# Kernel tuning notes

Measured on AMD Instinct MI355X. Metric: run time of the kernel, lower is better.

Reference implementation:

```python
import jax, jax.numpy as jnp
import numpy as np

B, L, NE, DOUT = 4, 4096, 64, 64
DI = 128          # backbone model dim (hardcoded d_inner in MambaDoc)
NL = 2            # num_layers
H = 2             # num_heads
N = 128           # state_dim
G = 1             # num_groups
CONV = 4          # conv_size
DIN = 2 * DI      # expand=2 -> 256 inner channels of the mixer
P = DIN // H      # headdim = 128
CCH = DIN + 2 * G * N      # 512 conv channels (x, B, C)
DPROJ = 2 * DIN + 2 * G * N + H  # 770 in_proj output width


def setup_inputs() -> dict:
    key = jax.random.key(0)
    ks = jax.random.split(key, 8)
    s = lambda k, shape, sc: (jax.random.normal(k, shape, jnp.float32) * sc)
    return {
        "x": s(ks[0], (B, L, NE), 1.0),
        "in_w": s(ks[1], (DI, NE), (1.0 / NE) ** 0.5),
        "in_b": jnp.zeros((DI,), jnp.float32),
        "out_w": s(ks[2], (DOUT, DI), (1.0 / DI) ** 0.5),
        "out_b": jnp.zeros((DOUT,), jnp.float32),
        "l_rms_w": jnp.ones((NL, DI), jnp.float32),
        "l_in_w": s(ks[3], (NL, DPROJ, DI), (1.0 / DI) ** 0.5),
        "conv_w": s(ks[4], (NL, CCH, CONV), (1.0 / CONV) ** 0.5),
        "conv_b": jnp.zeros((NL, CCH), jnp.float32),
        "dt_bias": s(ks[5], (NL, H), 0.1),
        "A_log": jnp.zeros((NL, H), jnp.float32),   # A = -exp(A_log) = -1
        "D_p": jnp.ones((NL, H), jnp.float32),
        "gnorm_w": jnp.ones((NL, DIN), jnp.float32),
        "l_out_w": s(ks[6], (NL, DI, DIN), (1.0 / DIN) ** 0.5),
        "fnorm_w": jnp.ones((DI,), jnp.float32),
    }


def _rms(x, w, eps=1e-5):
    return x * jax.lax.rsqrt(jnp.mean(x * x, -1, keepdims=True) + eps) * w


def _mamba_layer(x, rms_w, in_w, cw, cb, dtb, a_log, d, gnw, ow):
    # x: (B,L,DI)
    h = _rms(x, rms_w)
    zxbcdt = jnp.einsum("bld,ed->ble", h, in_w)  # (B,L,770)
    z, xBC, dt = jnp.split(zxbcdt, [DIN, DIN + CCH], axis=-1)
    # causal depthwise conv over time, conv_size taps
    xp = jnp.pad(xBC, ((0, 0), (CONV - 1, 0), (0, 0)))
    xc = cb + sum(xp[:, k:k + L, :] * cw[:, k] for k in range(CONV))
    xc = jax.nn.silu(xc)
    xs, Bm, Cm = jnp.split(xc, [DIN, DIN + G * N], axis=-1)
    xs = xs.reshape(B, L, H, P)
    dt = jax.nn.softplus(dt + dtb)                 # (B,L,H)
    dA = jnp.exp(dt * (-jnp.exp(a_log)))           # (B,L,H) discrete decay

    def step(hc, inp):
        dA_t, dt_t, x_t, B_t, C_t = inp  # (B,H),(B,H),(B,H,P),(B,N),(B,N)
        hc = hc * dA_t[:, :, None, None] + (dt_t[:, :, None] * x_t)[..., None] * B_t[:, None, None, :]
        y = jnp.einsum("bhpn,bn->bhp", hc, C_t)
        return hc, y

    h0 = jnp.zeros((B, H, P, N), x.dtype)
    seq = (jnp.moveaxis(dA, 1, 0), jnp.moveaxis(dt, 1, 0), jnp.moveaxis(xs, 1, 0),
           jnp.moveaxis(Bm, 1, 0), jnp.moveaxis(Cm, 1, 0))
    _, ys = jax.lax.scan(step, h0, seq)
    y = jnp.moveaxis(ys, 0, 1)                     # (B,L,H,P)
    y = y + xs * d[None, None, :, None]            # D skip connection
    y = _rms(y.reshape(B, L, DIN) * jax.nn.silu(z), gnw)  # gated RMSNorm
    return x + jnp.einsum("ble,de->bld", y, ow)


def reference(x, in_w, in_b, out_w, out_b, l_rms_w, l_in_w, conv_w, conv_b,
              dt_bias, A_log, D_p, gnorm_w, l_out_w, fnorm_w):
    xp = jnp.einsum("bln,dn->bld", x, in_w) + in_b
    h = xp
    for i in range(NL):
        h = _mamba_layer(h, l_rms_w[i], l_in_w[i], conv_w[i], conv_b[i],
                         dt_bias[i], A_log[i], D_p[i], gnorm_w[i], l_out_w[i])
    h = _rms(h, fnorm_w)            # backbone final norm
    out = xp + h                    # outer residual in MambaDoc.forward
    return jnp.einsum("bld,od->blo", out, out_w) + out_b
```

## Files before the change

### kernel.cpp

```cpp
#include <hip/hip_runtime.h>
#include <cstddef>
#include <cstdint>


#define LSEQ 4096
#define MTOK 16384

typedef unsigned short u16;
typedef _Float16 f16x8 __attribute__((ext_vector_type(8)));
typedef float f32x4 __attribute__((ext_vector_type(4)));

__device__ __forceinline__ u16 f2h(float x) {
    return __builtin_bit_cast(u16, (_Float16)x);
}
__device__ __forceinline__ float h2f(u16 u) {
    return (float)__builtin_bit_cast(_Float16, u);
}
__device__ __forceinline__ float silu_f(float x) { return x / (1.f + __expf(-x)); }

__device__ __forceinline__ void async_lds16(const void* g, void* l) {
    __builtin_amdgcn_global_load_lds(
        (const __attribute__((address_space(1))) unsigned int*)g,
        (__attribute__((address_space(3))) unsigned int*)l, 16, 0, 0);
}

__device__ __forceinline__ void cvt16(
    const float* __restrict__ in, u16* __restrict__ out, int g)
{
    float4 v = *(const float4*)&in[(size_t)g * 4];
    union { u16 u[4]; uint2 q; } pk;
    pk.u[0] = f2h(v.x); pk.u[1] = f2h(v.y);
    pk.u[2] = f2h(v.z); pk.u[3] = f2h(v.w);
    *(uint2*)&out[(size_t)g * 4] = pk.q;
}

__global__ __launch_bounds__(256) void cvt_all_kernel(
    const float* __restrict__ x, u16* __restrict__ xh,
    const float* __restrict__ in_w, u16* __restrict__ in_w16,
    const float* __restrict__ l_in_w, u16* __restrict__ l_in_w16,
    const float* __restrict__ l_out_w, u16* __restrict__ l_out_w16,
    const float* __restrict__ out_w, u16* __restrict__ out_w16)
{
    int g = blockIdx.x * 256 + threadIdx.x;
    if (g < 262144) { cvt16(x, xh, g); return; }
    g -= 262144;
    if (g < 2048) { cvt16(in_w, in_w16, g); return; }
    g -= 2048;
    if (g < 49280) { cvt16(l_in_w, l_in_w16, g); return; }
    g -= 49280;
    if (g < 16384) { cvt16(l_out_w, l_out_w16, g); return; }
    g -= 16384;
    if (g < 2048) { cvt16(out_w, out_w16, g); return; }
}

__global__ __launch_bounds__(256) void gemm_inproj_kernel(
    const u16* __restrict__ A, const u16* __restrict__ W,
    u16* __restrict__ zx16, float* __restrict__ dtb, float* __restrict__ Sb,
    const float* __restrict__ dt_bias, const float* __restrict__ A_log)
{
    __shared__ u16 sA[128 * 64];
    __shared__ u16 sW[128 * 64];
    __shared__ float sdt[2][128];
    const int K = 128, N = 770;
    const int n0 = blockIdx.x * 128, m0 = blockIdx.y * 128;
    const int tid = threadIdx.x, wid = tid >> 6, lane = tid & 63;
    const int wm = (wid >> 1) * 64, wn = (wid & 1) * 64;
    const int quad = lane >> 4, cl = lane & 15;
    f32x4 acc[4][4];
    #pragma unroll
    for (int i = 0; i < 4; i++)
        #pragma unroll
        for (int j = 0; j < 4; j++) acc[i][j] = f32x4{0.f, 0.f, 0.f, 0.f};

    for (int k0 = 0; k0 < K; k0 += 64) {
        #pragma unroll
        for (int i = 0; i < 4; i++) {
            int ck = i * 256 + tid;
            int r = ck >> 3, cc = ck & 7;
            int csw = (cc ^ (r & 7)) << 3;
            async_lds16(A + (size_t)(m0 + r) * K + k0 + csw,
                        (void*)(sA + (i * 256 + (tid & ~63)) * 8));
            int rr = n0 + r; if (rr >= N) rr = N - 1;
            async_lds16(W + (size_t)rr * K + k0 + csw,
                        (void*)(sW + (i * 256 + (tid & ~63)) * 8));
        }
        __syncthreads();
        #pragma unroll
        for (int ks = 0; ks < 2; ks++) {
            f16x8 af[4], wf[4];
            int kc = ks * 4 + quad;
            #pragma unroll
            for (int i = 0; i < 4; i++) {
                int r = wm + i * 16 + cl;
                af[i] = *(const f16x8*)&sA[r * 64 + ((kc ^ (r & 7)) << 3)];
            }
            #pragma unroll
            for (int j = 0; j < 4; j++) {
                int r = wn + j * 16 + cl;
                wf[j] = *(const f16x8*)&sW[r * 64 + ((kc ^ (r & 7)) << 3)];
            }
            #pragma unroll
            for (int i = 0; i < 4; i++)
                #pragma unroll
                for (int j = 0; j < 4; j++)
                    acc[i][j] = __builtin_amdgcn_mfma_f32_16x16x32_f16(
                        af[i], wf[j], acc[i][j], 0, 0, 0);
        }
        __syncthreads();
    }
    if (blockIdx.x < 6) {
        #pragma unroll
        for (int i = 0; i < 4; i++) {
            int m = m0 + wm + i * 16 + quad * 4;
            #pragma unroll
            for (int j = 0; j < 4; j++) {
                int n = n0 + wn + j * 16 + cl;
                #pragma unroll
                for (int r = 0; r < 4; r++)
                    zx16[(size_t)(m + r) * 768 + n] = f2h(acc[i][j][r]);
            }
        }
    } else {
        if ((wid & 1) == 0 && cl < 2) {
            #pragma unroll
            for (int i = 0; i < 4; i++)
                #pragma unroll
                for (int r = 0; r < 4; r++)
                    sdt[cl][wm + i * 16 + quad * 4 + r] = acc[i][0][r];
        }
        __syncthreads();
        const int hh = tid >> 7, t = tid & 127;
        float raw = sdt[hh][t] + dt_bias[hh];
        float dt = fmaxf(raw, 0.f) + log1pf(__expf(-fabsf(raw)));
        dtb[(size_t)(m0 + t) * 2 + hh] = dt;
        float ad = -__expf(A_log[hh]) * dt;
        __syncthreads();
        sdt[hh][t] = ad;
        __syncthreads();
        for (int off = 1; off < 128; off <<= 1) {
            float add = (t >= off) ? sdt[hh][t - off] : 0.f;
            __syncthreads();
            sdt[hh][t] += add;
            __syncthreads();
        }
        Sb[(size_t)(m0 + t) * 2 + hh] = sdt[hh][t];
    }
}

__global__ __launch_bounds__(256) void gemm128_rms_kernel(
    const u16* __restrict__ A, const u16* __restrict__ W,
    const float* __restrict__ bias, const float* __restrict__ rmsw,
    float* __restrict__ xp, float* __restrict__ hbuf,
    u16* __restrict__ hn, int K, int mode)
{
    __shared__ u16 sA[64 * 64];
    __shared__ u16 sW[128 * 64];
    __shared__ float red[64][33];
    __shared__ float srstd[64];
    const int m0 = blockIdx.y * 64;
    const int tid = threadIdx.x, wid = tid >> 6, lane = tid & 63;
    const int wm = (wid >> 1) * 32, wn = (wid & 1) * 64;
    const int quad = lane >> 4, cl = lane & 15;
    f32x4 acc[2][4];
    #pragma unroll
    for (int i = 0; i < 2; i++)
        #pragma unroll
        for (int j = 0; j < 4; j++) acc[i][j] = f32x4{0.f, 0.f, 0.f, 0.f};

    for (int k0 = 0; k0 < K; k0 += 64) {
        #pragma unroll
        for (int i = 0; i < 2; i++) {
            int ck = i * 256 + tid;
            int r = ck >> 3, cc = ck & 7;
            int csw = (cc ^ (r & 7)) << 3;
            async_lds16(A + (size_t)(m0 + r) * K + k0 + csw,
                        (void*)(sA + (i * 256 + (tid & ~63)) * 8));
        }
        #pragma unroll
        for (int i = 0; i < 4; i++) {
            int ck = i * 256 + tid;
            int r = ck >> 3, cc = ck & 7;
            int csw = (cc ^ (r & 7)) << 3;
            async_lds16(W + (size_t)r * K + k0 + csw,
                        (void*)(sW + (i * 256 + (tid & ~63)) * 8));
        }
        __syncthreads();
        #pragma unroll
        for (int ks = 0; ks < 2; ks++) {
            f16x8 af[2], wf[4];
            int kc = ks * 4 + quad;
            #pragma unroll
            for (int i = 0; i < 2; i++) {
                int r = wm + i * 16 + cl;
                af[i] = *(const f16x8*)&sA[r * 64 + ((kc ^ (r & 7)) << 3)];
            }
            #pragma unroll
            for (int j = 0; j < 4; j++) {
                int r = wn + j * 16 + cl;
                wf[j] = *(const f16x8*)&sW[r * 64 + ((kc ^ (r & 7)) << 3)];
            }
            #pragma unroll
            for (int i = 0; i < 2; i++)
                #pragma unroll
                for (int j = 0; j < 4; j++)
                    acc[i][j] = __builtin_amdgcn_mfma_f32_16x16x32_f16(
                        af[i], wf[j], acc[i][j], 0, 0, 0);
        }
        __syncthreads();
    }
    const int slot = (wid & 1) * 16 + cl;
    #pragma unroll
    for (int i = 0; i < 2; i++) {
        #pragma unroll
        for (int r = 0; r < 4; r++) {
            int t = wm + i * 16 + quad * 4 + r;
            size_t ob = (size_t)(m0 + t) * 128;
            float ssp = 0.f;
            #pragma unroll
            for (int j = 0; j < 4; j++) {
                int n = wn + j * 16 + cl;
                float v = acc[i][j][r];
                if (mode == 0) v += bias[n];
                else v += hbuf[ob + n];
                acc[i][j][r] = v;
                ssp += v * v;
            }
            red[t][slot] = ssp;
        }
    }
    __syncthreads();
    if (tid < 64) {
        float s = 0.f;
        #pragma unroll
        for (int sl = 0; sl < 32; sl++) s += red[tid][sl];
        srstd[tid] = rsqrtf(s * (1.f / 128.f) + 1e-5f);
    }
    __syncthreads();
    #pragma unroll
    for (int i = 0; i < 2; i++) {
        #pragma unroll
        for (int r = 0; r < 4; r++) {
            int t = wm + i * 16 + quad * 4 + r;
            size_t ob = (size_t)(m0 + t) * 128;
            u16* row = hn + (size_t)(m0 + t) * 128;
            float rstd = srstd[t];
            #pragma unroll
            for (int j = 0; j < 4; j++) {
                int n = wn + j * 16 + cl;
                float v = acc[i][j][r];
                if (mode == 0) { xp[ob + n] = v; hbuf[ob + n] = v; }
                else if (mode == 1) hbuf[ob + n] = v;
                float val = v * rstd * rmsw[n];
                if (mode == 2) val += xp[ob + n];
                row[n] = f2h(val);
            }
        }
    }
}

__global__ __launch_bounds__(256) void gemm_final_kernel(
    const u16* __restrict__ A, const u16* __restrict__ W,
    float* __restrict__ out, const float* __restrict__ bias)
{
    __shared__ u16 sA[64 * 64];
    __shared__ u16 sW[64 * 64];
    const int K = 128;
    const int m0 = blockIdx.y * 64;
    const int tid = threadIdx.x, wid = tid >> 6, lane = tid & 63;
    const int wm = (wid >> 1) * 32, wn = (wid & 1) * 32;
    const int quad = lane >> 4, cl = lane & 15;
    f32x4 acc[2][2];
    #pragma unroll
    for (int i = 0; i < 2; i++)
        #pragma unroll
        for (int j = 0; j < 2; j++) acc[i][j] = f32x4{0.f, 0.f, 0.f, 0.f};

    for (int k0 = 0; k0 < K; k0 += 64) {
        #pragma unroll
        for (int i = 0; i < 2; i++) {
            int ck = i * 256 + tid;
            int r = ck >> 3, cc = ck & 7;
            int csw = (cc ^ (r & 7)) << 3;
            async_lds16(A + (size_t)(m0 + r) * K + k0 + csw,
                        (void*)(sA + (i * 256 + (tid & ~63)) * 8));
            async_lds16(W + (size_t)r * K + k0 + csw,
                        (void*)(sW + (i * 256 + (tid & ~63)) * 8));
        }
        __syncthreads();
        #pragma unroll
        for (int ks = 0; ks < 2; ks++) {
            f16x8 af[2], wf[2];
            int kc = ks * 4 + quad;
            #pragma unroll
            for (int i = 0; i < 2; i++) {
                int r = wm + i * 16 + cl;
                af[i] = *(const f16x8*)&sA[r * 64 + ((kc ^ (r & 7)) << 3)];
            }
            #pragma unroll
            for (int j = 0; j < 2; j++) {
                int r = wn + j * 16 + cl;
                wf[j] = *(const f16x8*)&sW[r * 64 + ((kc ^ (r & 7)) << 3)];
            }
            #pragma unroll
            for (int i = 0; i < 2; i++)
                #pragma unroll
                for (int j = 0; j < 2; j++)
                    acc[i][j] = __builtin_amdgcn_mfma_f32_16x16x32_f16(
                        af[i], wf[j], acc[i][j], 0, 0, 0);
        }
        __syncthreads();
    }
    #pragma unroll
    for (int i = 0; i < 2; i++) {
        int m = m0 + wm + i * 16 + quad * 4;
        #pragma unroll
        for (int j = 0; j < 2; j++) {
            int n = wn + j * 16 + cl;
            float bv = bias[n];
            #pragma unroll
            for (int r = 0; r < 4; r++)
                out[(size_t)(m + r) * 64 + n] = acc[i][j][r] + bv;
        }
    }
}

__global__ __launch_bounds__(256) void conv_tile_kernel(
    const u16* __restrict__ zx16, const float* __restrict__ cw,
    const float* __restrict__ cb, const float* __restrict__ dtb,
    const float* __restrict__ Sb, u16* __restrict__ xc,
    u16* __restrict__ xT, u16* __restrict__ bT)
{
    __shared__ float sZ[67][68];
    __shared__ float sT[64][65];
    __shared__ float sw[2][64];
    const int tid = threadIdx.x;
    const int tok0 = blockIdx.x * 64;
    const int cg = blockIdx.y;
    const int cgb = cg * 64;
    const int l0 = tok0 & (LSEQ - 1);
    for (int idx = tid; idx < 67 * 16; idx += 256) {
        int row = idx >> 4, c4 = (idx & 15) * 4;
        int lr = l0 + row - 3;
        union { u16 u[4]; uint2 q; } ld;
        ld.q = make_uint2(0u, 0u);
        if (lr >= 0)
            ld.q = *(const uint2*)&zx16[(size_t)(tok0 + row - 3) * 768 + 256 + cgb + c4];
        #pragma unroll
        for (int j = 0; j < 4; j++) sZ[row][c4 + j] = h2f(ld.u[j]);
    }
    if ((cg == 4 || cg == 5) && tid < 128) {
        int hh = tid >> 6, j = tid & 63;
        int tokL = (tok0 & ~127) + 127;
        sw[hh][j] = __expf(Sb[(size_t)tokL * 2 + hh] - Sb[(size_t)(tok0 + j) * 2 + hh])
                    * dtb[(size_t)(tok0 + j) * 2 + hh];
    }
    const int ch = tid & 63;
    const int chg = cgb + ch;
    const float w0 = cw[chg * 4], w1 = cw[chg * 4 + 1];
    const float w2 = cw[chg * 4 + 2], w3 = cw[chg * 4 + 3];
    const float cbv = cb[chg];
    __syncthreads();
    #pragma unroll
    for (int k = 0; k < 16; k++) {
        int tokr = k * 4 + (tid >> 6);
        float a = cbv + sZ[tokr][ch] * w0 + sZ[tokr + 1][ch] * w1
                + sZ[tokr + 2][ch] * w2 + sZ[tokr + 3][ch] * w3;
        float v = silu_f(a);
        xc[(size_t)(tok0 + tokr) * 512 + chg] = f2h(v);
        sT[ch][tokr] = v;
    }
    __syncthreads();
    const int b = tok0 >> 12;
    const int c = (tok0 & (LSEQ - 1)) >> 7;
    const int s0 = tok0 & 127;
    if (cg < 4) {
        int hh = cg >> 1;
        int pbase = (cg & 1) * 64;
        u16* base = xT + (((size_t)((b * 2 + hh) * 32 + c)) << 14);
        for (int idx = tid; idx < 512; idx += 256) {
            int pr = idx >> 3, sc = (idx & 7) * 8;
            union { u16 u[8]; uint4 q; } pk;
            #pragma unroll
            for (int j = 0; j < 8; j++) pk.u[j] = f2h(sT[pr][sc + j]);
            *(uint4*)&base[(size_t)(pbase + pr) * 128 + s0 + sc] = pk.q;
        }
    } else if (cg < 6) {
        int nbase = (cg - 4) * 64;
        for (int hh = 0; hh < 2; hh++) {
            u16* base = bT + (((size_t)((b * 2 + hh) * 32 + c)) << 14);
            for (int idx = tid; idx < 512; idx += 256) {
                int nr = idx >> 3, sc = (idx & 7) * 8;
                union { u16 u[8]; uint4 q; } pk;
                #pragma unroll
                for (int j = 0; j < 8; j++)
                    pk.u[j] = f2h(sT[nr][sc + j] * sw[hh][sc + j]);
                *(uint4*)&base[(size_t)(nbase + nr) * 128 + s0 + sc] = pk.q;
            }
        }
    }
}

__global__ __launch_bounds__(256) void chunkstate_kernel(
    const u16* __restrict__ xT, const u16* __restrict__ bT,
    u16* __restrict__ Hb)
{
    __shared__ u16 sX[128 * 128];
    __shared__ u16 sB[128 * 128];
    const int c = blockIdx.x, h = blockIdx.y, b = blockIdx.z;
    const int tid = threadIdx.x, wid = tid >> 6, lane = tid & 63;
    const size_t blk = ((size_t)((b * 2 + h) * 32 + c)) << 14;
    #pragma unroll
    for (int i = 0; i < 8; i++) {
        int ck = i * 256 + tid;
        int r = ck >> 4, cc = ck & 15;
        size_t g = (size_t)r * 128 + ((cc ^ (r & 15)) << 3);
        async_lds16(xT + blk + g, (void*)(sX + (i * 256 + (tid & ~63)) * 8));
        async_lds16(bT + blk + g, (void*)(sB + (i * 256 + (tid & ~63)) * 8));
    }
    __syncthreads();
    const int wm = (wid >> 1) * 64, wn = (wid & 1) * 64;
    const int quad = lane >> 4, cl = lane & 15;
    f32x4 acc[4][4];
    #pragma unroll
    for (int i = 0; i < 4; i++)
        #pragma unroll
        for (int j = 0; j < 4; j++) acc[i][j] = f32x4{0.f, 0.f, 0.f, 0.f};
    #pragma unroll
    for (int ks = 0; ks < 4; ks++) {
        f16x8 xa[4], bb[4];
        int kc = ks * 4 + quad;
        #pragma unroll
        for (int i = 0; i < 4; i++) {
            int r = wm + i * 16 + cl;
            xa[i] = *(const f16x8*)&sX[r * 128 + ((kc ^ (r & 15)) << 3)];
        }
        #pragma unroll
        for (int j = 0; j < 4; j++) {
            int r = wn + j * 16 + cl;
            bb[j] = *(const f16x8*)&sB[r * 128 + ((kc ^ (r & 15)) << 3)];
        }
        #pragma unroll
        for (int i = 0; i < 4; i++)
            #pragma unroll
            for (int j = 0; j < 4; j++)
                acc[i][j] = __builtin_amdgcn_mfma_f32_16x16x32_f16(
                    xa[i], bb[j], acc[i][j], 0, 0, 0);
    }
    u16* out = Hb + blk;
    #pragma unroll
    for (int i = 0; i < 4; i++)
        #pragma unroll
        for (int j = 0; j < 4; j++)
            #pragma unroll
            for (int r = 0; r < 4; r++)
                out[(size_t)(wm + i * 16 + quad * 4 + r) * 128 + wn + j * 16 + cl]
                    = f2h(acc[i][j][r]);
}

__global__ __launch_bounds__(256) void statecombine_kernel(
    const float* __restrict__ Sb, const u16* __restrict__ Hb,
    u16* __restrict__ Hbf)
{
    const int e = blockIdx.x * 256 + threadIdx.x;
    const int h = blockIdx.y, b = blockIdx.z;
    const size_t base = ((size_t)((b * 2 + h) * 32)) << 14;
    float state = 0.f;
    for (int c = 0; c < 32; c++) {
        size_t idx = base + ((size_t)c << 14) + e;
        float v = h2f(Hb[idx]);
        Hbf[idx] = f2h(state);
        float dec = __expf(Sb[(size_t)(b * LSEQ + c * 128 + 127) * 2 + h]);
        state = dec * state + v;
    }
}

__global__ __launch_bounds__(512, 2) void ssd_fused_kernel(
    const u16* __restrict__ xc, const u16* __restrict__ xT,
    const u16* __restrict__ Hbf, const float* __restrict__ dtb,
    const float* __restrict__ Sb, const u16* __restrict__ zx16,
    const float* __restrict__ gnw, const float* __restrict__ Dp,
    u16* __restrict__ y16)
{
    __shared__ u16 bufCW[2][128 * 128];
    __shared__ u16 bufH[2][128 * 128];
    __shared__ float sS[2][128], sdt[2][128];
    __shared__ float red[128][5];
    __shared__ float srstd[128];
    const int c = blockIdx.x, b = blockIdx.y;
    const int tid = threadIdx.x, wid = tid >> 6, lane = tid & 63;
    const int quad = lane >> 4, cl = lane & 15;
    const int tok0 = b * LSEQ + c * 128;
    const size_t blk0 = ((size_t)((b * 2 + 0) * 32 + c)) << 14;
    const size_t blk1 = ((size_t)((b * 2 + 1) * 32 + c)) << 14;
    #pragma unroll
    for (int i = 0; i < 4; i++) {
        int ck = i * 512 + tid;
        int r = ck >> 4, cc = ck & 15;
        int csw = (cc ^ (r & 15)) << 3;
        int ldst = (i * 512 + (tid & ~63)) * 8;
        async_lds16(xc + (size_t)(tok0 + r) * 512 + 384 + csw, (void*)(&bufCW[0][0] + ldst));
        async_lds16(xc + (size_t)(tok0 + r) * 512 + 256 + csw, (void*)(&bufCW[1][0] + ldst));
        async_lds16(Hbf + blk0 + (size_t)r * 128 + csw, (void*)(&bufH[0][0] + ldst));
        async_lds16(Hbf + blk1 + (size_t)r * 128 + csw, (void*)(&bufH[1][0] + ldst));
    }
    if (tid < 256) {
        int hh = tid >> 7, t = tid & 127;
        sS[hh][t] = Sb[(size_t)(tok0 + t) * 2 + hh];
        sdt[hh][t] = dtb[(size_t)(tok0 + t) * 2 + hh];
    }
    __syncthreads();
    const int h = wid >> 2, w2 = wid & 3;
    const int wm = (w2 >> 1) * 64, wn = (w2 & 1) * 64;
    f32x4 acc[4][4];
    #pragma unroll
    for (int i = 0; i < 4; i++)
        #pragma unroll
        for (int j = 0; j < 4; j++) acc[i][j] = f32x4{0.f, 0.f, 0.f, 0.f};
    #pragma unroll
    for (int ks = 0; ks < 4; ks++) {
        f16x8 ca[4], hb[4];
        int kc = ks * 4 + quad;
        #pragma unroll
        for (int i = 0; i < 4; i++) {
            int r = wm + i * 16 + cl;
            ca[i] = *(const f16x8*)&bufCW[0][r * 128 + ((kc ^ (r & 15)) << 3)];
        }
        #pragma unroll
        for (int j = 0; j < 4; j++) {
            int r = wn + j * 16 + cl;
            hb[j] = *(const f16x8*)&bufH[h][r * 128 + ((kc ^ (r & 15)) << 3)];
        }
        #pragma unroll
        for (int i = 0; i < 4; i++)
            #pragma unroll
            for (int j = 0; j < 4; j++)
                acc[i][j] = __builtin_amdgcn_mfma_f32_16x16x32_f16(
                    ca[i], hb[j], acc[i][j], 0, 0, 0);
    }
    #pragma unroll
    for (int i = 0; i < 4; i++)
        #pragma unroll
        for (int r = 0; r < 4; r++) {
            float e = __expf(sS[h][wm + i * 16 + quad * 4 + r]);
            #pragma unroll
            for (int j = 0; j < 4; j++) acc[i][j][r] *= e;
        }
    const int sm0 = (wid >> 1) * 32, sn0 = (wid & 1) * 64;
    f32x4 sacc[2][4];
    #pragma unroll
    for (int i = 0; i < 2; i++)
        #pragma unroll
        for (int j = 0; j < 4; j++) sacc[i][j] = f32x4{0.f, 0.f, 0.f, 0.f};
    #pragma unroll
    for (int ks = 0; ks < 4; ks++) {
        f16x8 cs[2], bs[4];
        int kc = ks * 4 + quad;
        #pragma unroll
        for (int i2 = 0; i2 < 2; i2++) {
            int r = sm0 + i2 * 16 + cl;
            cs[i2] = *(const f16x8*)&bufCW[0][r * 128 + ((kc ^ (r & 15)) << 3)];
        }
        #pragma unroll
        for (int j = 0; j < 4; j++) {
            int r = sn0 + j * 16 + cl;
            bs[j] = *(const f16x8*)&bufCW[1][r * 128 + ((kc ^ (r & 15)) << 3)];
        }
        #pragma unroll
        for (int i2 = 0; i2 < 2; i2++)
            #pragma unroll
            for (int j = 0; j < 4; j++)
                if (sm0 + i2 * 16 + 15 >= sn0 + j * 16)
                    sacc[i2][j] = __builtin_amdgcn_mfma_f32_16x16x32_f16(
                        cs[i2], bs[j], sacc[i2][j], 0, 0, 0);
    }
    __syncthreads();
    #pragma unroll
    for (int i = 0; i < 4; i++) {
        int ck = i * 512 + tid;
        int r = ck >> 4, cc = ck & 15;
        int csw = (cc ^ (r & 15)) << 3;
        int ldst = (i * 512 + (tid & ~63)) * 8;
        async_lds16(xT + blk0 + (size_t)r * 128 + csw, (void*)(&bufH[0][0] + ldst));
        async_lds16(xT + blk1 + (size_t)r * 128 + csw, (void*)(&bufH[1][0] + ldst));
    }
    #pragma unroll
    for (int hh = 0; hh < 2; hh++)
        #pragma unroll
        for (int i2 = 0; i2 < 2; i2++)
            #pragma unroll
            for (int r = 0; r < 4; r++) {
                int t = sm0 + i2 * 16 + quad * 4 + r;
                float Stv = sS[hh][t];
                #pragma unroll
                for (int j = 0; j < 4; j++) {
                    int s = sn0 + j * 16 + cl;
                    float gv = 0.f;
                    if (s <= t)
                        gv = sacc[i2][j][r] * __expf(Stv - sS[hh][s]) * sdt[hh][s];
                    bufCW[hh][t * 128 + (((s >> 3) ^ (t & 15)) << 3) + (s & 7)] = f2h(gv);
                }
            }
    __syncthreads();
    #pragma unroll
    for (int ks = 0; ks < 4; ks++) {
        f16x8 ga[4], xb[4];
        int kc = ks * 4 + quad;
        #pragma unroll
        for (int i = 0; i < 4; i++) {
            int r = wm + i * 16 + cl;
            ga[i] = *(const f16x8*)&bufCW[h][r * 128 + ((kc ^ (r & 15)) << 3)];
        }
        #pragma unroll
        for (int j = 0; j < 4; j++) {
            int r = wn + j * 16 + cl;
            xb[j] = *(const f16x8*)&bufH[h][r * 128 + ((kc ^ (r & 15)) << 3)];
        }
        #pragma unroll
        for (int i = 0; i < 4; i++)
            #pragma unroll
            for (int j = 0; j < 4; j++)
                acc[i][j] = __builtin_amdgcn_mfma_f32_16x16x32_f16(
                    ga[i], xb[j], acc[i][j], 0, 0, 0);
    }
    const float dco = Dp[h];
    #pragma unroll
    for (int i = 0; i < 4; i++)
        #pragma unroll
        for (int r = 0; r < 4; r++) {
            int t = wm + i * 16 + quad * 4 + r;
            float ssp = 0.f;
            #pragma unroll
            for (int j = 0; j < 4; j++) {
                int p = wn + j * 16 + cl;
                float xv = h2f(bufH[h][p * 128 + (((t >> 3) ^ (p & 15)) << 3) + (t & 7)]);
                float zv = h2f(zx16[(size_t)(tok0 + t) * 768 + h * 128 + p]);
                float g = (acc[i][j][r] + dco * xv) * silu_f(zv);
                acc[i][j][r] = g;
                ssp += g * g;
            }
            ssp += __shfl_xor(ssp, 1);
            ssp += __shfl_xor(ssp, 2);
            ssp += __shfl_xor(ssp, 4);
            ssp += __shfl_xor(ssp, 8);
            if (cl == 0) red[t][h * 2 + (wn >> 6)] = ssp;
        }
    __syncthreads();
    if (tid < 128)
        srstd[tid] = rsqrtf((red[tid][0] + red[tid][1] + red[tid][2] + red[tid][3])
                            * (1.f / 256.f) + 1e-5f);
    __syncthreads();
    #pragma unroll
    for (int i = 0; i < 4; i++)
        #pragma unroll
        for (int r = 0; r < 4; r++) {
            int t = wm + i * 16 + quad * 4 + r;
            float rstd = srstd[t];
            u16* row = y16 + (size_t)(tok0 + t) * 256;
            #pragma unroll
            for (int j = 0; j < 4; j++) {
                int p = wn + j * 16 + cl;
                int e = h * 128 + p;
                row[e] = f2h(acc[i][j][r] * rstd * gnw[e]);
            }
        }
}

extern "C" void kernel_launch(void* const* d_in, const int* in_sizes, int n_in,
                              void* d_out, int out_size, void* d_ws, size_t ws_size,
                              hipStream_t stream)
{
    (void)in_sizes; (void)n_in; (void)out_size; (void)ws_size;
    const float* x       = (const float*)d_in[0];
    const float* in_w    = (const float*)d_in[1];
    const float* in_b    = (const float*)d_in[2];
    const float* out_w   = (const float*)d_in[3];
    const float* out_b   = (const float*)d_in[4];
    const float* l_rms_w = (const float*)d_in[5];
    const float* l_in_w  = (const float*)d_in[6];
    const float* conv_w  = (const float*)d_in[7];
    const float* conv_b  = (const float*)d_in[8];
    const float* dt_bias = (const float*)d_in[9];
    const float* A_log   = (const float*)d_in[10];
    const float* D_p     = (const float*)d_in[11];
    const float* gnorm_w = (const float*)d_in[12];
    const float* l_out_w = (const float*)d_in[13];
    const float* fnorm_w = (const float*)d_in[14];

    char* w = (char*)d_ws;
    float* xp    = (float*)(w);
    float* hbuf  = (float*)(w + 8388608);
    u16*   xh    = (u16*)(w + 16777216);
    u16*   hn16  = (u16*)(w + 18874368);
    u16*   zx16  = (u16*)(w + 23068672);
    float* dtb   = (float*)(w + 48234496);
    float* Sb    = (float*)(w + 48365568);
    u16*   Hb    = (u16*)(w + 48496640);
    u16*   xc    = (u16*)(w + 56885248);
    u16*   xT    = (u16*)(w + 73662464);
    u16*   bT    = (u16*)(w + 82051072);
    u16*   Hbf   = (u16*)(w + 90439680);
    u16*   y16   = (u16*)(w + 98828288);
    u16*   w16   = (u16*)(w + 107216896);
    u16* in_w16    = w16;
    u16* l_in_w16  = w16 + 8192;
    u16* l_out_w16 = w16 + 8192 + 197120;
    u16* out_w16   = w16 + 8192 + 197120 + 65536;

    cvt_all_kernel<<<1297, 256, 0, stream>>>(
        x, xh, in_w, in_w16, l_in_w, l_in_w16, l_out_w, l_out_w16,
        out_w, out_w16);

    gemm128_rms_kernel<<<dim3(1, 256), 256, 0, stream>>>(
        xh, in_w16, in_b, l_rms_w, xp, hbuf, hn16, 64, 0);

    for (int i = 0; i < 2; i++) {
        gemm_inproj_kernel<<<dim3(7, 128), 256, 0, stream>>>(
            hn16, l_in_w16 + (size_t)i * 770 * 128, zx16, dtb, Sb,
            dt_bias + i * 2, A_log + i * 2);
        conv_tile_kernel<<<dim3(256, 8), 256, 0, stream>>>(
            zx16, conv_w + i * 2048, conv_b + i * 512, dtb, Sb, xc, xT, bT);
        chunkstate_kernel<<<dim3(32, 2, 4), 256, 0, stream>>>(xT, bT, Hb);
        statecombine_kernel<<<dim3(64, 2, 4), 256, 0, stream>>>(Sb, Hb, Hbf);
        ssd_fused_kernel<<<dim3(32, 4), 512, 0, stream>>>(
            xc, xT, Hbf, dtb, Sb, zx16, gnorm_w + i * 256, D_p + i * 2, y16);
        gemm128_rms_kernel<<<dim3(1, 256), 256, 0, stream>>>(
            y16, l_out_w16 + (size_t)i * 128 * 256, nullptr,
            (i == 0) ? (l_rms_w + 128) : fnorm_w, xp, hbuf, hn16, 256,
            (i == 0) ? 1 : 2);
    }

    gemm_final_kernel<<<dim3(1, 256), 256, 0, stream>>>(
        hn16, out_w16, (float*)d_out, out_b);
}
```

Measured before the change: 255.3 us.

## Fuse conversions, conv, and final GEMM into neighboring kernels; store residuals in fp16

Removes the standalone fp32-to-fp16 conversion kernel by converting x and weights on the fly inside the GEMM loaders. The causal conv is folded into the chunk-state and SSD kernels, so the separate conv pass and its xc/bT intermediates disappear. The final output projection is fused into the last out-proj/RMS kernel. The residual buffers xp and hbuf move from fp32 to fp16 to cut memory traffic. The cost is redundant weight conversion in every block, conv recomputation in two kernels, and lower residual precision.

```diff
diff --git a/kernel.cpp b/kernel.cpp
--- a/kernel.cpp
+++ b/kernel.cpp
@@ -24,37 +24,114 @@
         (__attribute__((address_space(3))) unsigned int*)l, 16, 0, 0);
 }
 
-__device__ __forceinline__ void cvt16(
-    const float* __restrict__ in, u16* __restrict__ out, int g)
+__device__ __forceinline__ uint4 cvt8(const float* __restrict__ src) {
+    float4 a = *(const float4*)src;
+    float4 b = *(const float4*)(src + 4);
+    union { u16 u[8]; uint4 q; } pk;
+    pk.u[0] = f2h(a.x); pk.u[1] = f2h(a.y); pk.u[2] = f2h(a.z); pk.u[3] = f2h(a.w);
+    pk.u[4] = f2h(b.x); pk.u[5] = f2h(b.y); pk.u[6] = f2h(b.z); pk.u[7] = f2h(b.w);
+    return pk.q;
+}
+
+__global__ __launch_bounds__(256) void gemm_rms0_kernel(
+    const float* __restrict__ xf, const float* __restrict__ wf,
+    const float* __restrict__ bias, const float* __restrict__ rmsw,
+    u16* __restrict__ xp16, u16* __restrict__ hbuf16, u16* __restrict__ hn16)
 {
-    float4 v = *(const float4*)&in[(size_t)g * 4];
-    union { u16 u[4]; uint2 q; } pk;
-    pk.u[0] = f2h(v.x); pk.u[1] = f2h(v.y);
-    pk.u[2] = f2h(v.z); pk.u[3] = f2h(v.w);
-    *(uint2*)&out[(size_t)g * 4] = pk.q;
-}
-
-__global__ __launch_bounds__(256) void cvt_all_kernel(
-    const float* __restrict__ x, u16* __restrict__ xh,
-    const float* __restrict__ in_w, u16* __restrict__ in_w16,
-    const float* __restrict__ l_in_w, u16* __restrict__ l_in_w16,
-    const float* __restrict__ l_out_w, u16* __restrict__ l_out_w16,
-    const float* __restrict__ out_w, u16* __restrict__ out_w16)
-{
-    int g = blockIdx.x * 256 + threadIdx.x;
-    if (g < 262144) { cvt16(x, xh, g); return; }
-    g -= 262144;
-    if (g < 2048) { cvt16(in_w, in_w16, g); return; }
-    g -= 2048;
-    if (g < 49280) { cvt16(l_in_w, l_in_w16, g); return; }
-    g -= 49280;
-    if (g < 16384) { cvt16(l_out_w, l_out_w16, g); return; }
-    g -= 16384;
-    if (g < 2048) { cvt16(out_w, out_w16, g); return; }
+    __shared__ u16 sA[64 * 64];
+    __shared__ u16 sW[128 * 64];
+    __shared__ float red[64][33];
+    __shared__ float srstd[64];
+    const int m0 = blockIdx.y * 64;
+    const int tid = threadIdx.x, wid = tid >> 6, lane = tid & 63;
+    const int wm = (wid >> 1) * 32, wn = (wid & 1) * 64;
+    const int quad = lane >> 4, cl = lane & 15;
+    #pragma unroll
+    for (int i = 0; i < 2; i++) {
+        int ck = i * 256 + tid;
+        int r = ck >> 3, cc = ck & 7;
+        int csw = (cc ^ (r & 7)) << 3;
+        *(uint4*)&sA[ck * 8] = cvt8(xf + (size_t)(m0 + r) * 64 + csw);
+    }
+    #pragma unroll
+    for (int i = 0; i < 4; i++) {
+        int ck = i * 256 + tid;
+        int r = ck >> 3, cc = ck & 7;
+        int csw = (cc ^ (r & 7)) << 3;
+        *(uint4*)&sW[ck * 8] = cvt8(wf + (size_t)r * 64 + csw);
+    }
+    __syncthreads();
+    f32x4 acc[2][4];
+    #pragma unroll
+    for (int i = 0; i < 2; i++)
+        #pragma unroll
+        for (int j = 0; j < 4; j++) acc[i][j] = f32x4{0.f, 0.f, 0.f, 0.f};
+    #pragma unroll
+    for (int ks = 0; ks < 2; ks++) {
+        f16x8 af[2], wv[4];
+        int kc = ks * 4 + quad;
+        #pragma unroll
+        for (int i = 0; i < 2; i++) {
+            int r = wm + i * 16 + cl;
+            af[i] = *(const f16x8*)&sA[r * 64 + ((kc ^ (r & 7)) << 3)];
+        }
+        #pragma unroll
+        for (int j = 0; j < 4; j++) {
+            int r = wn + j * 16 + cl;
+            wv[j] = *(const f16x8*)&sW[r * 64 + ((kc ^ (r & 7)) << 3)];
+        }
+        #pragma unroll
+        for (int i = 0; i < 2; i++)
+            #pragma unroll
+            for (int j = 0; j < 4; j++)
+                acc[i][j] = __builtin_amdgcn_mfma_f32_16x16x32_f16(
+                    af[i], wv[j], acc[i][j], 0, 0, 0);
+    }
+    const int slot = (wid & 1) * 16 + cl;
+    #pragma unroll
+    for (int i = 0; i < 2; i++)
+        #pragma unroll
+        for (int r = 0; r < 4; r++) {
+            int t = wm + i * 16 + quad * 4 + r;
+            float ssp = 0.f;
+            #pragma unroll
+            for (int j = 0; j < 4; j++) {
+                int n = wn + j * 16 + cl;
+                float v = acc[i][j][r] + bias[n];
+                acc[i][j][r] = v;
+                ssp += v * v;
+            }
+            red[t][slot] = ssp;
+        }
+    __syncthreads();
+    if (tid < 64) {
+        float s = 0.f;
+        #pragma unroll
+        for (int sl = 0; sl < 32; sl++) s += red[tid][sl];
+        srstd[tid] = rsqrtf(s * (1.f / 128.f) + 1e-5f);
+    }
+    __syncthreads();
+    #pragma unroll
+    for (int i = 0; i < 2; i++)
+        #pragma unroll
+        for (int r = 0; r < 4; r++) {
+            int t = wm + i * 16 + quad * 4 + r;
+            size_t ob = (size_t)(m0 + t) * 128;
+            float rstd = srstd[t];
+            #pragma unroll
+            for (int j = 0; j < 4; j++) {
+                int n = wn + j * 16 + cl;
+                float v = acc[i][j][r];
+                u16 vh = f2h(v);
+                xp16[ob + n] = vh;
+                hbuf16[ob + n] = vh;
+                hn16[ob + n] = f2h(v * rstd * rmsw[n]);
+            }
+        }
 }
 
 __global__ __launch_bounds__(256) void gemm_inproj_kernel(
-    const u16* __restrict__ A, const u16* __restrict__ W,
+    const u16* __restrict__ A, const float* __restrict__ Wf,
     u16* __restrict__ zx16, float* __restrict__ dtb, float* __restrict__ Sb,
     const float* __restrict__ dt_bias, const float* __restrict__ A_log)
 {
@@ -80,14 +157,19 @@
             int csw = (cc ^ (r & 7)) << 3;
             async_lds16(A + (size_t)(m0 + r) * K + k0 + csw,
                         (void*)(sA + (i * 256 + (tid & ~63)) * 8));
+        }
+        #pragma unroll
+        for (int i = 0; i < 4; i++) {
+            int ck = i * 256 + tid;
+            int r = ck >> 3, cc = ck & 7;
+            int csw = (cc ^ (r & 7)) << 3;
             int rr = n0 + r; if (rr >= N) rr = N - 1;
-            async_lds16(W + (size_t)rr * K + k0 + csw,
-                        (void*)(sW + (i * 256 + (tid & ~63)) * 8));
+            *(uint4*)&sW[ck * 8] = cvt8(Wf + (size_t)rr * K + k0 + csw);
         }
         __syncthreads();
         #pragma unroll
         for (int ks = 0; ks < 2; ks++) {
-            f16x8 af[4], wf[4];
+            f16x8 af[4], wv[4];
             int kc = ks * 4 + quad;
             #pragma unroll
             for (int i = 0; i < 4; i++) {
@@ -97,14 +179,14 @@
             #pragma unroll
             for (int j = 0; j < 4; j++) {
                 int r = wn + j * 16 + cl;
-                wf[j] = *(const f16x8*)&sW[r * 64 + ((kc ^ (r & 7)) << 3)];
+                wv[j] = *(const f16x8*)&sW[r * 64 + ((kc ^ (r & 7)) << 3)];
             }
             #pragma unroll
             for (int i = 0; i < 4; i++)
                 #pragma unroll
                 for (int j = 0; j < 4; j++)
                     acc[i][j] = __builtin_amdgcn_mfma_f32_16x16x32_f16(
-                        af[i], wf[j], acc[i][j], 0, 0, 0);
+                        af[i], wv[j], acc[i][j], 0, 0, 0);
         }
         __syncthreads();
     }
@@ -147,300 +229,133 @@
     }
 }
 
-__global__ __launch_bounds__(256) void gemm128_rms_kernel(
-    const u16* __restrict__ A, const u16* __restrict__ W,
-    const float* __restrict__ bias, const float* __restrict__ rmsw,
-    float* __restrict__ xp, float* __restrict__ hbuf,
-    u16* __restrict__ hn, int K, int mode)
-{
-    __shared__ u16 sA[64 * 64];
-    __shared__ u16 sW[128 * 64];
-    __shared__ float red[64][33];
-    __shared__ float srstd[64];
-    const int m0 = blockIdx.y * 64;
-    const int tid = threadIdx.x, wid = tid >> 6, lane = tid & 63;
-    const int wm = (wid >> 1) * 32, wn = (wid & 1) * 64;
-    const int quad = lane >> 4, cl = lane & 15;
-    f32x4 acc[2][4];
-    #pragma unroll
-    for (int i = 0; i < 2; i++)
-        #pragma unroll
-        for (int j = 0; j < 4; j++) acc[i][j] = f32x4{0.f, 0.f, 0.f, 0.f};
-
-    for (int k0 = 0; k0 < K; k0 += 64) {
-        #pragma unroll
-        for (int i = 0; i < 2; i++) {
-            int ck = i * 256 + tid;
-            int r = ck >> 3, cc = ck & 7;
-            int csw = (cc ^ (r & 7)) << 3;
-            async_lds16(A + (size_t)(m0 + r) * K + k0 + csw,
-                        (void*)(sA + (i * 256 + (tid & ~63)) * 8));
-        }
-        #pragma unroll
-        for (int i = 0; i < 4; i++) {
-            int ck = i * 256 + tid;
-            int r = ck >> 3, cc = ck & 7;
-            int csw = (cc ^ (r & 7)) << 3;
-            async_lds16(W + (size_t)r * K + k0 + csw,
-                        (void*)(sW + (i * 256 + (tid & ~63)) * 8));
-        }
-        __syncthreads();
-        #pragma unroll
-        for (int ks = 0; ks < 2; ks++) {
-            f16x8 af[2], wf[4];
-            int kc = ks * 4 + quad;
-            #pragma unroll
-            for (int i = 0; i < 2; i++) {
-                int r = wm + i * 16 + cl;
-                af[i] = *(const f16x8*)&sA[r * 64 + ((kc ^ (r & 7)) << 3)];
-            }
-            #pragma unroll
-            for (int j = 0; j < 4; j++) {
-                int r = wn + j * 16 + cl;
-                wf[j] = *(const f16x8*)&sW[r * 64 + ((kc ^ (r & 7)) << 3)];
-            }
-            #pragma unroll
-            for (int i = 0; i < 2; i++)
-                #pragma unroll
-                for (int j = 0; j < 4; j++)
-                    acc[i][j] = __builtin_amdgcn_mfma_f32_16x16x32_f16(
-                        af[i], wf[j], acc[i][j], 0, 0, 0);
-        }
-        __syncthreads();
-    }
-    const int slot = (wid & 1) * 16 + cl;
-    #pragma unroll
-    for (int i = 0; i < 2; i++) {
-        #pragma unroll
-        for (int r = 0; r < 4; r++) {
-            int t = wm + i * 16 + quad * 4 + r;
-            size_t ob = (size_t)(m0 + t) * 128;
-            float ssp = 0.f;
-            #pragma unroll
-            for (int j = 0; j < 4; j++) {
-                int n = wn + j * 16 + cl;
-                float v = acc[i][j][r];
-                if (mode == 0) v += bias[n];
-                else v += hbuf[ob + n];
-                acc[i][j][r] = v;
-                ssp += v * v;
-            }
-            red[t][slot] = ssp;
-        }
-    }
-    __syncthreads();
-    if (tid < 64) {
-        float s = 0.f;
-        #pragma unroll
-        for (int sl = 0; sl < 32; sl++) s += red[tid][sl];
-        srstd[tid] = rsqrtf(s * (1.f / 128.f) + 1e-5f);
-    }
-    __syncthreads();
-    #pragma unroll
-    for (int i = 0; i < 2; i++) {
-        #pragma unroll
-        for (int r = 0; r < 4; r++) {
-            int t = wm + i * 16 + quad * 4 + r;
-            size_t ob = (size_t)(m0 + t) * 128;
-            u16* row = hn + (size_t)(m0 + t) * 128;
-            float rstd = srstd[t];
-            #pragma unroll
-            for (int j = 0; j < 4; j++) {
-                int n = wn + j * 16 + cl;
-                float v = acc[i][j][r];
-                if (mode == 0) { xp[ob + n] = v; hbuf[ob + n] = v; }
-                else if (mode == 1) hbuf[ob + n] = v;
-                float val = v * rstd * rmsw[n];
-                if (mode == 2) val += xp[ob + n];
-                row[n] = f2h(val);
-            }
-        }
-    }
-}
-
-__global__ __launch_bounds__(256) void gemm_final_kernel(
-    const u16* __restrict__ A, const u16* __restrict__ W,
-    float* __restrict__ out, const float* __restrict__ bias)
-{
-    __shared__ u16 sA[64 * 64];
-    __shared__ u16 sW[64 * 64];
-    const int K = 128;
-    const int m0 = blockIdx.y * 64;
-    const int tid = threadIdx.x, wid = tid >> 6, lane = tid & 63;
-    const int wm = (wid >> 1) * 32, wn = (wid & 1) * 32;
-    const int quad = lane >> 4, cl = lane & 15;
-    f32x4 acc[2][2];
-    #pragma unroll
-    for (int i = 0; i < 2; i++)
-        #pragma unroll
-        for (int j = 0; j < 2; j++) acc[i][j] = f32x4{0.f, 0.f, 0.f, 0.f};
-
-    for (int k0 = 0; k0 < K; k0 += 64) {
-        #pragma unroll
-        for (int i = 0; i < 2; i++) {
-            int ck = i * 256 + tid;
-            int r = ck >> 3, cc = ck & 7;
-            int csw = (cc ^ (r & 7)) << 3;
-            async_lds16(A + (size_t)(m0 + r) * K + k0 + csw,
-                        (void*)(sA + (i * 256 + (tid & ~63)) * 8));
-            async_lds16(W + (size_t)r * K + k0 + csw,
-                        (void*)(sW + (i * 256 + (tid & ~63)) * 8));
-        }
-        __syncthreads();
-        #pragma unroll
-        for (int ks = 0; ks < 2; ks++) {
-            f16x8 af[2], wf[2];
-            int kc = ks * 4 + quad;
-            #pragma unroll
-            for (int i = 0; i < 2; i++) {
-                int r = wm + i * 16 + cl;
-                af[i] = *(const f16x8*)&sA[r * 64 + ((kc ^ (r & 7)) << 3)];
-            }
-            #pragma unroll
-            for (int j = 0; j < 2; j++) {
-                int r = wn + j * 16 + cl;
-                wf[j] = *(const f16x8*)&sW[r * 64 + ((kc ^ (r & 7)) << 3)];
-            }
-            #pragma unroll
-            for (int i = 0; i < 2; i++)
-                #pragma unroll
-                for (int j = 0; j < 2; j++)
-                    acc[i][j] = __builtin_amdgcn_mfma_f32_16x16x32_f16(
-                        af[i], wf[j], acc[i][j], 0, 0, 0);
-        }
-        __syncthreads();
-    }
-    #pragma unroll
-    for (int i = 0; i < 2; i++) {
-        int m = m0 + wm + i * 16 + quad * 4;
-        #pragma unroll
-        for (int j = 0; j < 2; j++) {
-            int n = wn + j * 16 + cl;
-            float bv = bias[n];
-            #pragma unroll
-            for (int r = 0; r < 4; r++)
-                out[(size_t)(m + r) * 64 + n] = acc[i][j][r] + bv;
-        }
-    }
-}
-
-__global__ __launch_bounds__(256) void conv_tile_kernel(
+__global__ __launch_bounds__(512) void chunkstate_conv_kernel(
     const u16* __restrict__ zx16, const float* __restrict__ cw,
     const float* __restrict__ cb, const float* __restrict__ dtb,
-    const float* __restrict__ Sb, u16* __restrict__ xc,
-    u16* __restrict__ xT, u16* __restrict__ bT)
+    const float* __restrict__ Sb, u16* __restrict__ xT, u16* __restrict__ Hb)
 {
-    __shared__ float sZ[67][68];
-    __shared__ float sT[64][65];
-    __shared__ float sw[2][64];
-    const int tid = threadIdx.x;
-    const int tok0 = blockIdx.x * 64;
-    const int cg = blockIdx.y;
-    const int cgb = cg * 64;
-    const int l0 = tok0 & (LSEQ - 1);
-    for (int idx = tid; idx < 67 * 16; idx += 256) {
-        int row = idx >> 4, c4 = (idx & 15) * 4;
-        int lr = l0 + row - 3;
-        union { u16 u[4]; uint2 q; } ld;
-        ld.q = make_uint2(0u, 0u);
-        if (lr >= 0)
-            ld.q = *(const uint2*)&zx16[(size_t)(tok0 + row - 3) * 768 + 256 + cgb + c4];
-        #pragma unroll
-        for (int j = 0; j < 4; j++) sZ[row][c4 + j] = h2f(ld.u[j]);
-    }
-    if ((cg == 4 || cg == 5) && tid < 128) {
-        int hh = tid >> 6, j = tid & 63;
-        int tokL = (tok0 & ~127) + 127;
-        sw[hh][j] = __expf(Sb[(size_t)tokL * 2 + hh] - Sb[(size_t)(tok0 + j) * 2 + hh])
-                    * dtb[(size_t)(tok0 + j) * 2 + hh];
-    }
-    const int ch = tid & 63;
-    const int chg = cgb + ch;
-    const float w0 = cw[chg * 4], w1 = cw[chg * 4 + 1];
-    const float w2 = cw[chg * 4 + 2], w3 = cw[chg * 4 + 3];
-    const float cbv = cb[chg];
-    __syncthreads();
-    #pragma unroll
-    for (int k = 0; k < 16; k++) {
-        int tokr = k * 4 + (tid >> 6);
-        float a = cbv + sZ[tokr][ch] * w0 + sZ[tokr + 1][ch] * w1
-                + sZ[tokr + 2][ch] * w2 + sZ[tokr + 3][ch] * w3;
-        float v = silu_f(a);
-        xc[(size_t)(tok0 + tokr) * 512 + chg] = f2h(v);
-        sT[ch][tokr] = v;
-    }
-    __syncthreads();
-    const int b = tok0 >> 12;
-    const int c = (tok0 & (LSEQ - 1)) >> 7;
-    const int s0 = tok0 & 127;
-    if (cg < 4) {
-        int hh = cg >> 1;
-        int pbase = (cg & 1) * 64;
-        u16* base = xT + (((size_t)((b * 2 + hh) * 32 + c)) << 14);
-        for (int idx = tid; idx < 512; idx += 256) {
-            int pr = idx >> 3, sc = (idx & 7) * 8;
-            union { u16 u[8]; uint4 q; } pk;
-            #pragma unroll
-            for (int j = 0; j < 8; j++) pk.u[j] = f2h(sT[pr][sc + j]);
-            *(uint4*)&base[(size_t)(pbase + pr) * 128 + s0 + sc] = pk.q;
-        }
-    } else if (cg < 6) {
-        int nbase = (cg - 4) * 64;
-        for (int hh = 0; hh < 2; hh++) {
-            u16* base = bT + (((size_t)((b * 2 + hh) * 32 + c)) << 14);
-            for (int idx = tid; idx < 512; idx += 256) {
-                int nr = idx >> 3, sc = (idx & 7) * 8;
-                union { u16 u[8]; uint4 q; } pk;
-                #pragma unroll
-                for (int j = 0; j < 8; j++)
-                    pk.u[j] = f2h(sT[nr][sc + j] * sw[hh][sc + j]);
-                *(uint4*)&base[(size_t)(nbase + nr) * 128 + s0 + sc] = pk.q;
-            }
-        }
-    }
-}
-
-__global__ __launch_bounds__(256) void chunkstate_kernel(
-    const u16* __restrict__ xT, const u16* __restrict__ bT,
-    u16* __restrict__ Hb)
-{
-    __shared__ u16 sX[128 * 128];
-    __shared__ u16 sB[128 * 128];
+    __shared__ u16 raw[2560 * 8];
+    __shared__ u16 XT[128 * 128];
+    __shared__ u16 BT[128 * 128];
+    __shared__ float scw[2][128][4];
+    __shared__ float scb[2][128];
+    __shared__ float ssw[128];
     const int c = blockIdx.x, h = blockIdx.y, b = blockIdx.z;
     const int tid = threadIdx.x, wid = tid >> 6, lane = tid & 63;
+    const int quad = lane >> 4, cl = lane & 15;
+    const int tok0 = b * LSEQ + c * 128;
+    for (int idx = tid; idx < 256; idx += 512) {
+        int grp = idx >> 7, j = idx & 127;
+        int ch = grp ? (256 + j) : (128 * h + j);
+        float4 w4 = *(const float4*)&cw[ch * 4];
+        scw[grp][j][0] = w4.x; scw[grp][j][1] = w4.y;
+        scw[grp][j][2] = w4.z; scw[grp][j][3] = w4.w;
+        scb[grp][j] = cb[ch];
+    }
+    if (tid < 128) {
+        float Sl = Sb[(size_t)(tok0 + 127) * 2 + h];
+        ssw[tid] = __expf(Sl - Sb[(size_t)(tok0 + tid) * 2 + h])
+                   * dtb[(size_t)(tok0 + tid) * 2 + h];
+    }
+    #pragma unroll
+    for (int i = 0; i < 5; i++) {
+        int ck = i * 512 + tid;
+        int r = ck >> 4; if (r > 130) r = 130;
+        int cc = ck & 15;
+        int tok = tok0 - 3 + r; if (tok < 0) tok = 0;
+        async_lds16(zx16 + (size_t)tok * 768 + 256 + 128 * h + ((cc ^ (r & 15)) << 3),
+                    (void*)(raw + (i * 512 + (tid & ~63)) * 8));
+    }
+    __syncthreads();
+    if (c == 0 && tid < 48) *(uint4*)&raw[tid * 8] = make_uint4(0, 0, 0, 0);
+    __syncthreads();
+    #pragma unroll
+    for (int it = 0; it < 4; it++) {
+        int idx = it * 512 + tid;
+        int s = idx & 127, pg = idx >> 7;
+        f16x8 v[4];
+        #pragma unroll
+        for (int k = 0; k < 4; k++) {
+            int rr = s + k;
+            v[k] = *(const f16x8*)&raw[rr * 128 + ((pg ^ (rr & 15)) << 3)];
+        }
+        #pragma unroll
+        for (int j = 0; j < 8; j++) {
+            int p = pg * 8 + j;
+            float o = scb[0][p] + (float)v[0][j] * scw[0][p][0]
+                    + (float)v[1][j] * scw[0][p][1]
+                    + (float)v[2][j] * scw[0][p][2]
+                    + (float)v[3][j] * scw[0][p][3];
+            o = silu_f(o);
+            XT[p * 128 + (((s >> 3) ^ (p & 15)) << 3) + (s & 7)] = f2h(o);
+        }
+    }
+    __syncthreads();
     const size_t blk = ((size_t)((b * 2 + h) * 32 + c)) << 14;
     #pragma unroll
-    for (int i = 0; i < 8; i++) {
-        int ck = i * 256 + tid;
+    for (int i = 0; i < 5; i++) {
+        int ck = i * 512 + tid;
+        int r = ck >> 4; if (r > 130) r = 130;
+        int cc = ck & 15;
+        int tok = tok0 - 3 + r; if (tok < 0) tok = 0;
+        async_lds16(zx16 + (size_t)tok * 768 + 512 + ((cc ^ (r & 15)) << 3),
+                    (void*)(raw + (i * 512 + (tid & ~63)) * 8));
+    }
+    #pragma unroll
+    for (int it = 0; it < 4; it++) {
+        int ck = it * 512 + tid;
         int r = ck >> 4, cc = ck & 15;
-        size_t g = (size_t)r * 128 + ((cc ^ (r & 15)) << 3);
-        async_lds16(xT + blk + g, (void*)(sX + (i * 256 + (tid & ~63)) * 8));
-        async_lds16(bT + blk + g, (void*)(sB + (i * 256 + (tid & ~63)) * 8));
-    }
-    __syncthreads();
-    const int wm = (wid >> 1) * 64, wn = (wid & 1) * 64;
-    const int quad = lane >> 4, cl = lane & 15;
-    f32x4 acc[4][4];
-    #pragma unroll
-    for (int i = 0; i < 4; i++)
+        uint4 q = *(const uint4*)&XT[r * 128 + ((cc ^ (r & 15)) << 3)];
+        *(uint4*)&xT[blk + (size_t)r * 128 + cc * 8] = q;
+    }
+    __syncthreads();
+    if (c == 0 && tid < 48) *(uint4*)&raw[tid * 8] = make_uint4(0, 0, 0, 0);
+    __syncthreads();
+    #pragma unroll
+    for (int it = 0; it < 4; it++) {
+        int idx = it * 512 + tid;
+        int s = idx & 127, ng = idx >> 7;
+        f16x8 v[4];
+        #pragma unroll
+        for (int k = 0; k < 4; k++) {
+            int rr = s + k;
+            v[k] = *(const f16x8*)&raw[rr * 128 + ((ng ^ (rr & 15)) << 3)];
+        }
+        float wsv = ssw[s];
+        #pragma unroll
+        for (int j = 0; j < 8; j++) {
+            int n = ng * 8 + j;
+            float o = scb[1][n] + (float)v[0][j] * scw[1][n][0]
+                    + (float)v[1][j] * scw[1][n][1]
+                    + (float)v[2][j] * scw[1][n][2]
+                    + (float)v[3][j] * scw[1][n][3];
+            o = silu_f(o) * wsv;
+            BT[n * 128 + (((s >> 3) ^ (n & 15)) << 3) + (s & 7)] = f2h(o);
+        }
+    }
+    __syncthreads();
+    const int wm = (wid >> 1) * 32, wn = (wid & 1) * 64;
+    f32x4 acc[2][4];
+    #pragma unroll
+    for (int i = 0; i < 2; i++)
         #pragma unroll
         for (int j = 0; j < 4; j++) acc[i][j] = f32x4{0.f, 0.f, 0.f, 0.f};
     #pragma unroll
     for (int ks = 0; ks < 4; ks++) {
-        f16x8 xa[4], bb[4];
+        f16x8 xa[2], bb[4];
         int kc = ks * 4 + quad;
         #pragma unroll
-        for (int i = 0; i < 4; i++) {
+        for (int i = 0; i < 2; i++) {
             int r = wm + i * 16 + cl;
-            xa[i] = *(const f16x8*)&sX[r * 128 + ((kc ^ (r & 15)) << 3)];
+            xa[i] = *(const f16x8*)&XT[r * 128 + ((kc ^ (r & 15)) << 3)];
         }
         #pragma unroll
         for (int j = 0; j < 4; j++) {
             int r = wn + j * 16 + cl;
-            bb[j] = *(const f16x8*)&sB[r * 128 + ((kc ^ (r & 15)) << 3)];
-        }
-        #pragma unroll
-        for (int i = 0; i < 4; i++)
+            bb[j] = *(const f16x8*)&BT[r * 128 + ((kc ^ (r & 15)) << 3)];
+        }
+        #pragma unroll
+        for (int i = 0; i < 2; i++)
             #pragma unroll
             for (int j = 0; j < 4; j++)
                 acc[i][j] = __builtin_amdgcn_mfma_f32_16x16x32_f16(
@@ -448,7 +363,7 @@
     }
     u16* out = Hb + blk;
     #pragma unroll
-    for (int i = 0; i < 4; i++)
+    for (int i = 0; i < 2; i++)
         #pragma unroll
         for (int j = 0; j < 4; j++)
             #pragma unroll
@@ -474,16 +389,18 @@
     }
 }
 
-__global__ __launch_bounds__(512, 2) void ssd_fused_kernel(
-    const u16* __restrict__ xc, const u16* __restrict__ xT,
+__global__ __launch_bounds__(512) void ssd_fused_conv_kernel(
+    const u16* __restrict__ zx16, const u16* __restrict__ xT,
     const u16* __restrict__ Hbf, const float* __restrict__ dtb,
-    const float* __restrict__ Sb, const u16* __restrict__ zx16,
-    const float* __restrict__ gnw, const float* __restrict__ Dp,
-    u16* __restrict__ y16)
+    const float* __restrict__ Sb, const float* __restrict__ cw,
+    const float* __restrict__ cb, const float* __restrict__ gnw,
+    const float* __restrict__ Dp, u16* __restrict__ y16)
 {
     __shared__ u16 bufCW[2][128 * 128];
     __shared__ u16 bufH[2][128 * 128];
     __shared__ float sS[2][128], sdt[2][128];
+    __shared__ float scw2[2][128][4];
+    __shared__ float scb2[2][128];
     __shared__ float red[128][5];
     __shared__ float srstd[128];
     const int c = blockIdx.x, b = blockIdx.y;
@@ -492,21 +409,98 @@
     const int tok0 = b * LSEQ + c * 128;
     const size_t blk0 = ((size_t)((b * 2 + 0) * 32 + c)) << 14;
     const size_t blk1 = ((size_t)((b * 2 + 1) * 32 + c)) << 14;
+    u16* scratch = &bufH[0][0];
+    for (int idx = tid; idx < 256; idx += 512) {
+        int grp = idx >> 7, j = idx & 127;
+        int ch = grp ? (256 + j) : (384 + j);
+        float4 w4 = *(const float4*)&cw[ch * 4];
+        scw2[grp][j][0] = w4.x; scw2[grp][j][1] = w4.y;
+        scw2[grp][j][2] = w4.z; scw2[grp][j][3] = w4.w;
+        scb2[grp][j] = cb[ch];
+    }
+    if (tid < 256) {
+        int hh = tid >> 7, t = tid & 127;
+        sS[hh][t] = Sb[(size_t)(tok0 + t) * 2 + hh];
+        sdt[hh][t] = dtb[(size_t)(tok0 + t) * 2 + hh];
+    }
+    #pragma unroll
+    for (int i = 0; i < 5; i++) {
+        int ck = i * 512 + tid;
+        int r = ck >> 4; if (r > 130) r = 130;
+        int cc = ck & 15;
+        int tok = tok0 - 3 + r; if (tok < 0) tok = 0;
+        async_lds16(zx16 + (size_t)tok * 768 + 640 + ((cc ^ (r & 15)) << 3),
+                    (void*)(scratch + (i * 512 + (tid & ~63)) * 8));
+    }
+    __syncthreads();
+    if (c == 0 && tid < 48) *(uint4*)&scratch[tid * 8] = make_uint4(0, 0, 0, 0);
+    __syncthreads();
+    #pragma unroll
+    for (int it = 0; it < 4; it++) {
+        int idx = it * 512 + tid;
+        int t = idx & 127, ng = idx >> 7;
+        f16x8 v[4];
+        #pragma unroll
+        for (int k = 0; k < 4; k++) {
+            int rr = t + k;
+            v[k] = *(const f16x8*)&scratch[rr * 128 + ((ng ^ (rr & 15)) << 3)];
+        }
+        union { u16 u[8]; uint4 q; } pk;
+        #pragma unroll
+        for (int j = 0; j < 8; j++) {
+            int n = ng * 8 + j;
+            float o = scb2[0][n] + (float)v[0][j] * scw2[0][n][0]
+                    + (float)v[1][j] * scw2[0][n][1]
+                    + (float)v[2][j] * scw2[0][n][2]
+                    + (float)v[3][j] * scw2[0][n][3];
+            pk.u[j] = f2h(silu_f(o));
+        }
+        *(uint4*)&bufCW[0][t * 128 + ((ng ^ (t & 15)) << 3)] = pk.q;
+    }
+    __syncthreads();
+    #pragma unroll
+    for (int i = 0; i < 5; i++) {
+        int ck = i * 512 + tid;
+        int r = ck >> 4; if (r > 130) r = 130;
+        int cc = ck & 15;
+        int tok = tok0 - 3 + r; if (tok < 0) tok = 0;
+        async_lds16(zx16 + (size_t)tok * 768 + 512 + ((cc ^ (r & 15)) << 3),
+                    (void*)(scratch + (i * 512 + (tid & ~63)) * 8));
+    }
+    __syncthreads();
+    if (c == 0 && tid < 48) *(uint4*)&scratch[tid * 8] = make_uint4(0, 0, 0, 0);
+    __syncthreads();
+    #pragma unroll
+    for (int it = 0; it < 4; it++) {
+        int idx = it * 512 + tid;
+        int t = idx & 127, ng = idx >> 7;
+        f16x8 v[4];
+        #pragma unroll
+        for (int k = 0; k < 4; k++) {
+            int rr = t + k;
+            v[k] = *(const f16x8*)&scratch[rr * 128 + ((ng ^ (rr & 15)) << 3)];
+        }
+        union { u16 u[8]; uint4 q; } pk;
+        #pragma unroll
+        for (int j = 0; j < 8; j++) {
+            int n = ng * 8 + j;
+            float o = scb2[1][n] + (float)v[0][j] * scw2[1][n][0]
+                    + (float)v[1][j] * scw2[1][n][1]
+                    + (float)v[2][j] * scw2[1][n][2]
+                    + (float)v[3][j] * scw2[1][n][3];
+            pk.u[j] = f2h(silu_f(o));
+        }
+        *(uint4*)&bufCW[1][t * 128 + ((ng ^ (t & 15)) << 3)] = pk.q;
+    }
+    __syncthreads();
     #pragma unroll
     for (int i = 0; i < 4; i++) {
         int ck = i * 512 + tid;
         int r = ck >> 4, cc = ck & 15;
         int csw = (cc ^ (r & 15)) << 3;
         int ldst = (i * 512 + (tid & ~63)) * 8;
-        async_lds16(xc + (size_t)(tok0 + r) * 512 + 384 + csw, (void*)(&bufCW[0][0] + ldst));
-        async_lds16(xc + (size_t)(tok0 + r) * 512 + 256 + csw, (void*)(&bufCW[1][0] + ldst));
         async_lds16(Hbf + blk0 + (size_t)r * 128 + csw, (void*)(&bufH[0][0] + ldst));
         async_lds16(Hbf + blk1 + (size_t)r * 128 + csw, (void*)(&bufH[1][0] + ldst));
-    }
-    if (tid < 256) {
-        int hh = tid >> 7, t = tid & 127;
-        sS[hh][t] = Sb[(size_t)(tok0 + t) * 2 + hh];
-        sdt[hh][t] = dtb[(size_t)(tok0 + t) * 2 + hh];
     }
     __syncthreads();
     const int h = wid >> 2, w2 = wid & 3;
@@ -663,6 +657,166 @@
                 row[e] = f2h(acc[i][j][r] * rstd * gnw[e]);
             }
         }
+}
+
+__global__ __launch_bounds__(256) void gemm_outrms_kernel(
+    const u16* __restrict__ A, const float* __restrict__ Wf,
+    const float* __restrict__ rmsw, u16* __restrict__ xp16,
+    u16* __restrict__ hbuf16, u16* __restrict__ hn16,
+    const float* __restrict__ out_wf, const float* __restrict__ out_b,
+    float* __restrict__ dout, int mode)
+{
+    __shared__ u16 sA[64 * 64];
+    __shared__ u16 sW[128 * 64];
+    __shared__ float red[64][33];
+    __shared__ float srstd[64];
+    __shared__ u16 hn2[64 * 128];
+    __shared__ u16 ow[64 * 128];
+    const int K = 256;
+    const int m0 = blockIdx.y * 64;
+    const int tid = threadIdx.x, wid = tid >> 6, lane = tid & 63;
+    const int wm = (wid >> 1) * 32, wn = (wid & 1) * 64;
+    const int quad = lane >> 4, cl = lane & 15;
+    f32x4 acc[2][4];
+    #pragma unroll
+    for (int i = 0; i < 2; i++)
+        #pragma unroll
+        for (int j = 0; j < 4; j++) acc[i][j] = f32x4{0.f, 0.f, 0.f, 0.f};
+
+    for (int k0 = 0; k0 < K; k0 += 64) {
+        #pragma unroll
+        for (int i = 0; i < 2; i++) {
+            int ck = i * 256 + tid;
+            int r = ck >> 3, cc = ck & 7;
+            int csw = (cc ^ (r & 7)) << 3;
+            async_lds16(A + (size_t)(m0 + r) * K + k0 + csw,
+                        (void*)(sA + (i * 256 + (tid & ~63)) * 8));
+        }
+        #pragma unroll
+        for (int i = 0; i < 4; i++) {
+            int ck = i * 256 + tid;
+            int r = ck >> 3, cc = ck & 7;
+            int csw = (cc ^ (r & 7)) << 3;
+            *(uint4*)&sW[ck * 8] = cvt8(Wf + (size_t)r * K + k0 + csw);
+        }
+        __syncthreads();
+        #pragma unroll
+        for (int ks = 0; ks < 2; ks++) {
+            f16x8 af[2], wv[4];
+            int kc = ks * 4 + quad;
+            #pragma unroll
+            for (int i = 0; i < 2; i++) {
+                int r = wm + i * 16 + cl;
+                af[i] = *(const f16x8*)&sA[r * 64 + ((kc ^ (r & 7)) << 3)];
+            }
+            #pragma unroll
+            for (int j = 0; j < 4; j++) {
+                int r = wn + j * 16 + cl;
+                wv[j] = *(const f16x8*)&sW[r * 64 + ((kc ^ (r & 7)) << 3)];
+            }
+            #pragma unroll
+            for (int i = 0; i < 2; i++)
+                #pragma unroll
+                for (int j = 0; j < 4; j++)
+                    acc[i][j] = __builtin_amdgcn_mfma_f32_16x16x32_f16(
+                        af[i], wv[j], acc[i][j], 0, 0, 0);
+        }
+        __syncthreads();
+    }
+    const int slot = (wid & 1) * 16 + cl;
+    #pragma unroll
+    for (int i = 0; i < 2; i++)
+        #pragma unroll
+        for (int r = 0; r < 4; r++) {
+            int t = wm + i * 16 + quad * 4 + r;
+            size_t ob = (size_t)(m0 + t) * 128;
+            float ssp = 0.f;
+            #pragma unroll
+            for (int j = 0; j < 4; j++) {
+                int n = wn + j * 16 + cl;
+                float v = acc[i][j][r] + h2f(hbuf16[ob + n]);
+                acc[i][j][r] = v;
+                ssp += v * v;
+            }
+            red[t][slot] = ssp;
+        }
+    __syncthreads();
+    if (tid < 64) {
+        float s = 0.f;
+        #pragma unroll
+        for (int sl = 0; sl < 32; sl++) s += red[tid][sl];
+        srstd[tid] = rsqrtf(s * (1.f / 128.f) + 1e-5f);
+    }
+    __syncthreads();
+    #pragma unroll
+    for (int i = 0; i < 2; i++)
+        #pragma unroll
+        for (int r = 0; r < 4; r++) {
+            int t = wm + i * 16 + quad * 4 + r;
+            size_t ob = (size_t)(m0 + t) * 128;
+            float rstd = srstd[t];
+            #pragma unroll
+            for (int j = 0; j < 4; j++) {
+                int n = wn + j * 16 + cl;
+                float v = acc[i][j][r];
+                float val = v * rstd * rmsw[n];
+                if (mode == 1) {
+                    hbuf16[ob + n] = f2h(v);
+                    hn16[ob + n] = f2h(val);
+                } else {
+                    val += h2f(xp16[ob + n]);
+                    hn2[t * 128 + (((n >> 3) ^ (t & 15)) << 3) + (n & 7)] = f2h(val);
+                }
+            }
+        }
+    if (mode == 1) return;
+    #pragma unroll
+    for (int i = 0; i < 4; i++) {
+        int ck = i * 256 + tid;
+        int rr = ck >> 4, cc = ck & 15;
+        int csw = (cc ^ (rr & 15)) << 3;
+        *(uint4*)&ow[ck * 8] = cvt8(out_wf + (size_t)rr * 128 + csw);
+    }
+    __syncthreads();
+    const int wm4 = (wid >> 1) * 32, wn4 = (wid & 1) * 32;
+    f32x4 acc2[2][2];
+    #pragma unroll
+    for (int i = 0; i < 2; i++)
+        #pragma unroll
+        for (int j = 0; j < 2; j++) acc2[i][j] = f32x4{0.f, 0.f, 0.f, 0.f};
+    #pragma unroll
+    for (int ks = 0; ks < 4; ks++) {
+        f16x8 af2[2], wf2[2];
+        int kc = ks * 4 + quad;
+        #pragma unroll
+        for (int i = 0; i < 2; i++) {
+            int r = wm4 + i * 16 + cl;
+            af2[i] = *(const f16x8*)&hn2[r * 128 + ((kc ^ (r & 15)) << 3)];
+        }
+        #pragma unroll
+        for (int j = 0; j < 2; j++) {
+            int rr = wn4 + j * 16 + cl;
+            wf2[j] = *(const f16x8*)&ow[rr * 128 + ((kc ^ (rr & 15)) << 3)];
+        }
+        #pragma unroll
+        for (int i = 0; i < 2; i++)
+            #pragma unroll
+            for (int j = 0; j < 2; j++)
+                acc2[i][j] = __builtin_amdgcn_mfma_f32_16x16x32_f16(
+                    af2[i], wf2[j], acc2[i][j], 0, 0, 0);
+    }
+    #pragma unroll
+    for (int i = 0; i < 2; i++) {
+        int m = m0 + wm4 + i * 16 + quad * 4;
+        #pragma unroll
+        for (int j = 0; j < 2; j++) {
+            int n = wn4 + j * 16 + cl;
+            float bv = out_b[n];
+            #pragma unroll
+            for (int r = 0; r < 4; r++)
+                dout[(size_t)(m + r) * 64 + n] = acc2[i][j][r] + bv;
+        }
+    }
 }
 
 extern "C" void kernel_launch(void* const* d_in, const int* in_sizes, int n_in,
@@ -687,48 +841,33 @@
     const float* fnorm_w = (const float*)d_in[14];
 
     char* w = (char*)d_ws;
-    float* xp    = (float*)(w);
-    float* hbuf  = (float*)(w + 8388608);
-    u16*   xh    = (u16*)(w + 16777216);
-    u16*   hn16  = (u16*)(w + 18874368);
-    u16*   zx16  = (u16*)(w + 23068672);
-    float* dtb   = (float*)(w + 48234496);
-    float* Sb    = (float*)(w + 48365568);
-    u16*   Hb    = (u16*)(w + 48496640);
-    u16*   xc    = (u16*)(w + 56885248);
-    u16*   xT    = (u16*)(w + 73662464);
-    u16*   bT    = (u16*)(w + 82051072);
-    u16*   Hbf   = (u16*)(w + 90439680);
-    u16*   y16   = (u16*)(w + 98828288);
-    u16*   w16   = (u16*)(w + 107216896);
-    u16* in_w16    = w16;
-    u16* l_in_w16  = w16 + 8192;
-    u16* l_out_w16 = w16 + 8192 + 197120;
-    u16* out_w16   = w16 + 8192 + 197120 + 65536;
-
-    cvt_all_kernel<<<1297, 256, 0, stream>>>(
-        x, xh, in_w, in_w16, l_in_w, l_in_w16, l_out_w, l_out_w16,
-        out_w, out_w16);
-
-    gemm128_rms_kernel<<<dim3(1, 256), 256, 0, stream>>>(
-        xh, in_w16, in_b, l_rms_w, xp, hbuf, hn16, 64, 0);
+    u16*   xp16   = (u16*)(w);
+    u16*   hbuf16 = (u16*)(w + 4194304);
+    u16*   hn16   = (u16*)(w + 8388608);
+    u16*   zx16   = (u16*)(w + 12582912);
+    float* dtb    = (float*)(w + 37748736);
+    float* Sb     = (float*)(w + 37879808);
+    u16*   Hb     = (u16*)(w + 38010880);
+    u16*   Hbf    = (u16*)(w + 46399488);
+    u16*   xT     = (u16*)(w + 54788096);
+    u16*   y16    = (u16*)(w + 63176704);
+
+    gemm_rms0_kernel<<<dim3(1, 256), 256, 0, stream>>>(
+        x, in_w, in_b, l_rms_w, xp16, hbuf16, hn16);
 
     for (int i = 0; i < 2; i++) {
         gemm_inproj_kernel<<<dim3(7, 128), 256, 0, stream>>>(
-            hn16, l_in_w16 + (size_t)i * 770 * 128, zx16, dtb, Sb,
+            hn16, l_in_w + (size_t)i * 770 * 128, zx16, dtb, Sb,
             dt_bias + i * 2, A_log + i * 2);
-        conv_tile_kernel<<<dim3(256, 8), 256, 0, stream>>>(
-            zx16, conv_w + i * 2048, conv_b + i * 512, dtb, Sb, xc, xT, bT);
-        chunkstate_kernel<<<dim3(32, 2, 4), 256, 0, stream>>>(xT, bT, Hb);
+        chunkstate_conv_kernel<<<dim3(32, 2, 4), 512, 0, stream>>>(
+            zx16, conv_w + i * 2048, conv_b + i * 512, dtb, Sb, xT, Hb);
         statecombine_kernel<<<dim3(64, 2, 4), 256, 0, stream>>>(Sb, Hb, Hbf);
-        ssd_fused_kernel<<<dim3(32, 4), 512, 0, stream>>>(
-            xc, xT, Hbf, dtb, Sb, zx16, gnorm_w + i * 256, D_p + i * 2, y16);
-        gemm128_rms_kernel<<<dim3(1, 256), 256, 0, stream>>>(
-            y16, l_out_w16 + (size_t)i * 128 * 256, nullptr,
-            (i == 0) ? (l_rms_w + 128) : fnorm_w, xp, hbuf, hn16, 256,
-            (i == 0) ? 1 : 2);
-    }
-
-    gemm_final_kernel<<<dim3(1, 256), 256, 0, stream>>>(
-        hn16, out_w16, (float*)d_out, out_b);
-}
+        ssd_fused_conv_kernel<<<dim3(32, 4), 512, 0, stream>>>(
+            zx16, xT, Hbf, dtb, Sb, conv_w + i * 2048, conv_b + i * 512,
+            gnorm_w + i * 256, D_p + i * 2, y16);
+        gemm_outrms_kernel<<<dim3(1, 256), 256, 0, stream>>>(
+            y16, l_out_w + (size_t)i * 128 * 256,
+            (i == 0) ? (l_rms_w + 128) : fnorm_w, xp16, hbuf16, hn16,
+            out_w, out_b, (float*)d_out, (i == 0) ? 1 : 3);
+    }
+}
```

Measured after the change: 246.2 us. 1.04x faster.
